# Kernel tuning notes

Hardware: AMD Instinct MI355X
Metric: run time of the kernel (lower is better)

## Reference

```python
import jax, jax.numpy as jnp
import numpy as np

Q_H, KV_H, DIM = 32, 8, 4096
HEAD_DIM = DIM // Q_H
FACTOR = Q_H // KV_H
BS, SL = 2, 2048


def setup_inputs() -> dict:
    key = jax.random.key(0)
    ks = jax.random.split(key, 9)
    s_in = 1.0 / np.sqrt(DIM)
    x = jax.random.normal(ks[0], (BS, SL, DIM), dtype=jnp.float32)
    wq_w = jax.random.uniform(ks[1], (DIM, Q_H * HEAD_DIM), jnp.float32, -s_in, s_in)
    wq_b = jax.random.uniform(ks[2], (Q_H * HEAD_DIM,), jnp.float32, -s_in, s_in)
    wk_w = jax.random.uniform(ks[3], (DIM, KV_H * HEAD_DIM), jnp.float32, -s_in, s_in)
    wk_b = jax.random.uniform(ks[4], (KV_H * HEAD_DIM,), jnp.float32, -s_in, s_in)
    wv_w = jax.random.uniform(ks[5], (DIM, KV_H * HEAD_DIM), jnp.float32, -s_in, s_in)
    wv_b = jax.random.uniform(ks[6], (KV_H * HEAD_DIM,), jnp.float32, -s_in, s_in)
    wo_w = jax.random.uniform(ks[7], (DIM, DIM), jnp.float32, -s_in, s_in)
    wo_b = jax.random.uniform(ks[8], (DIM,), jnp.float32, -s_in, s_in)
    return {"x": x, "wq_w": wq_w, "wq_b": wq_b, "wk_w": wk_w, "wk_b": wk_b,
            "wv_w": wv_w, "wv_b": wv_b, "wo_w": wo_w, "wo_b": wo_b}


def reference(x, wq_w, wq_b, wk_w, wk_b, wv_w, wv_b, wo_w, wo_b):
    bs, sl, _ = x.shape
    # projections
    q = (x @ wq_w + wq_b).reshape(bs, sl, Q_H, HEAD_DIM)          # [b,s,Hq,d]
    k = (x @ wk_w + wk_b).reshape(bs, sl, KV_H, HEAD_DIM)         # [b,s,Hkv,d]
    v = (x @ wv_w + wv_b).reshape(bs, sl, KV_H, HEAD_DIM)
    # group queries by kv head: [b,s,Hkv,factor,d]
    qg = q.reshape(bs, sl, KV_H, FACTOR, HEAD_DIM)
    scale = 1.0 / jnp.sqrt(jnp.asarray(HEAD_DIM, x.dtype))
    # scores: broadcast kv heads instead of physically repeating
    attn = jnp.einsum('bqhfd,bkhd->bhfqk', qg, k) * scale          # [b,Hkv,f,Sq,Sk]
    att = jax.nn.softmax(attn, axis=-1)
    a = jnp.einsum('bhfqk,bkhd->bqhfd', att, v)                    # [b,Sq,Hkv,f,d]
    a = a.reshape(bs, sl, DIM)
    return a @ wo_w + wo_b
```

## Files before the change

kernel.cpp:

```cpp
#include <hip/hip_runtime.h>
#include <math.h>


typedef unsigned short u16;
typedef unsigned int u32;
typedef __bf16 bf16x8 __attribute__((ext_vector_type(8)));
typedef float f32x4 __attribute__((ext_vector_type(4)));
typedef float f32x16 __attribute__((ext_vector_type(16)));
typedef unsigned short u16x8 __attribute__((ext_vector_type(8)));
typedef unsigned short u16x4 __attribute__((ext_vector_type(4)));
typedef int i32x2 __attribute__((ext_vector_type(2)));

#define MFMA16(a, b, c) __builtin_amdgcn_mfma_f32_16x16x32_bf16((a), (b), (c), 0, 0, 0)
#define MFMA32(a, b, c) __builtin_amdgcn_mfma_f32_32x32x16_bf16((a), (b), (c), 0, 0, 0)

#define GLDS(gp, lp)                                                      \
  __builtin_amdgcn_global_load_lds(                                       \
      (const __attribute__((address_space(1))) unsigned int*)(gp),        \
      (__attribute__((address_space(3))) unsigned int*)(lp), 16, 0, 0)

__device__ __forceinline__ u16 f2b(float f) {
  unsigned b = __float_as_uint(f);
  b += 0x7fffu + ((b >> 16) & 1u);
  return (u16)(b >> 16);
}

__device__ __forceinline__ u32 pk2(float a, float b) {
  union { __bf16 h[2]; u32 w; } u;
  u.h[0] = (__bf16)a;
  u.h[1] = (__bf16)b;
  return u.w;
}

__global__ __launch_bounds__(256) void cast_f32_bf16(const float* __restrict__ in,
                                                     u16* __restrict__ out, int n) {
  int i = (blockIdx.x * 256 + threadIdx.x) * 8;
  if (i >= n) return;
  f32x4 a = *(const f32x4*)&in[i];
  f32x4 b = *(const f32x4*)&in[i + 4];
  u16x8 v;
#pragma unroll
  for (int j = 0; j < 4; j++) { v[j] = f2b(a[j]); v[4 + j] = f2b(b[j]); }
  *(u16x8*)&out[i] = v;
}

__global__ __launch_bounds__(256) void transpose_cast(const float* __restrict__ in,
                                                      u16* __restrict__ out,
                                                      int R, int C) {
  __shared__ u16 t[32][33];
  const int lc = threadIdx.x & 31;
  const int lr = threadIdx.x >> 5;
  const int c0 = blockIdx.x * 32, r0 = blockIdx.y * 32;
#pragma unroll
  for (int i = 0; i < 4; i++) {
    int r = lr + i * 8;
    t[r][lc] = f2b(in[(size_t)(r0 + r) * C + c0 + lc]);
  }
  __syncthreads();
#pragma unroll
  for (int i = 0; i < 4; i++) {
    int r = lr + i * 8;
    out[(size_t)(c0 + r) * R + r0 + lc] = t[lc][r];
  }
}

template <int STORE_T, int OUT_F32>
__global__ __launch_bounds__(256, 2) void gemm_bt(const u16* __restrict__ A,
                                                  const u16* __restrict__ BT,
                                                  const float* __restrict__ bias,
                                                  void* __restrict__ Cv,
                                                  int M, int N) {
  __shared__ u16 As[128][64];
  __shared__ u16 Bs[128][64];
  const int tid = threadIdx.x;
  const int lane = tid & 63, wave = tid >> 6;
  const int l15 = lane & 15, quad = lane >> 4;
  const int m0 = blockIdx.y * 128, n0 = blockIdx.x * 128;
  const int wm = (wave >> 1) * 64, wn = (wave & 1) * 64;
  const int srow = wave * 32 + (lane >> 3);
  const int scol = (lane & 7) * 8;
  const u16* gA = &A[(size_t)(m0 + srow) * 4096 + scol];
  const u16* gB = &BT[(size_t)(n0 + srow) * 4096 + scol];
  f32x4 acc[4][4] = {};
  for (int kb = 0; kb < 4096; kb += 64) {
    __syncthreads();
#pragma unroll
    for (int j = 0; j < 4; j++) {
      GLDS(gA + (size_t)j * 8 * 4096 + kb, &As[wave * 32 + j * 8][0]);
      GLDS(gB + (size_t)j * 8 * 4096 + kb, &Bs[wave * 32 + j * 8][0]);
    }
    __syncthreads();
#pragma unroll
    for (int ks = 0; ks < 2; ks++) {
      bf16x8 a[4], b[4];
#pragma unroll
      for (int mt = 0; mt < 4; mt++)
        a[mt] = *(const bf16x8*)&As[wm + mt * 16 + l15][ks * 32 + quad * 8];
#pragma unroll
      for (int nt = 0; nt < 4; nt++)
        b[nt] = *(const bf16x8*)&Bs[wn + nt * 16 + l15][ks * 32 + quad * 8];
#pragma unroll
      for (int mt = 0; mt < 4; mt++)
#pragma unroll
        for (int nt = 0; nt < 4; nt++)
          acc[mt][nt] = MFMA16(a[mt], b[nt], acc[mt][nt]);
    }
  }
  float bv[4];
#pragma unroll
  for (int nt = 0; nt < 4; nt++) bv[nt] = bias[n0 + wn + nt * 16 + l15];
#pragma unroll
  for (int mt = 0; mt < 4; mt++) {
    const int row = m0 + wm + mt * 16 + quad * 4;
#pragma unroll
    for (int nt = 0; nt < 4; nt++) {
      const int col = n0 + wn + nt * 16 + l15;
      if (STORE_T) {
        u16x4 v;
#pragma unroll
        for (int r = 0; r < 4; r++) v[r] = f2b(acc[mt][nt][r] + bv[nt]);
        *(u16x4*)&((u16*)Cv)[(size_t)col * M + row] = v;
      } else if (OUT_F32) {
#pragma unroll
        for (int r = 0; r < 4; r++)
          ((float*)Cv)[(size_t)(row + r) * N + col] = acc[mt][nt][r] + bv[nt];
      } else {
#pragma unroll
        for (int r = 0; r < 4; r++)
          ((u16*)Cv)[(size_t)(row + r) * N + col] = f2b(acc[mt][nt][r] + bv[nt]);
      }
    }
  }
}

#define STAGE_K(bf, t)                                                         \
  {                                                                            \
    _Pragma("unroll") for (int i_ = 0; i_ < 4; i_++)                           \
      GLDS(gK + (size_t)((t) * 64 + i_ * 4) * 1024 + (offK ^ ((i_ & 1) << 5)), \
           &KsB[bf][(wave * 16 + i_ * 4) * 128]);                              \
  }
#define STAGE_V(t)                                                             \
  {                                                                            \
    _Pragma("unroll") for (int i_ = 0; i_ < 4; i_++)                           \
      GLDS(gV + (size_t)(i_ * 8) * 4096 + (t) * 64,                            \
           &Vs[(wave * 32 + i_ * 8) * 64]);                                    \
  }

__global__ __launch_bounds__(256, 3) void flash_gqa(const u16* __restrict__ K,
                                                    const u16* __restrict__ VT,
                                                    u16* __restrict__ QO) {
  __shared__ __align__(16) u16 KsB[2][64 * 128];
  __shared__ __align__(16) u16 Vs[128 * 64];
  const int tid = threadIdx.x;
  const int lane = tid & 63, wave = tid >> 6;
  const int l31 = lane & 31, hi = lane >> 5;
  const int bx = blockIdx.x;
  const int qt = bx & 15, h = (bx >> 4) & 31, b = bx >> 9;
  const int hk = h >> 2;
  const int qrow0 = b * 2048 + qt * 128 + wave * 32;
  const float scl2 = 0.08838834764831845f * 1.4426950408889634f;

  const int offK = ((lane & 15) * 8) ^ ((lane >> 4) << 3);
  const u16* gK = &K[(size_t)(b * 2048 + wave * 16 + (lane >> 4)) * 1024 + hk * 128];
  const u16* gV = &VT[(size_t)(hk * 128 + wave * 32 + (lane >> 3)) * 4096 + b * 2048 +
                      (((lane & 7) * 8) ^ ((lane >> 3) << 3))];

  STAGE_K(0, 0);

  bf16x8 qf[8];
#pragma unroll
  for (int ks = 0; ks < 8; ks++)
    qf[ks] = *(const bf16x8*)&QO[(size_t)(qrow0 + l31) * 4096 + h * 128 + ks * 16 + hi * 8];

  f32x16 o[4] = {};
  float mrun = -3.0e38f, lrun = 0.0f;

  __syncthreads();

  for (int t = 0; t < 32; t++) {
    const int bf = t & 1;
    STAGE_V(t);
    if (t < 31) STAGE_K(bf ^ 1, t + 1);

    f32x16 st[2] = {};
    __builtin_amdgcn_s_setprio(1);
#pragma unroll
    for (int ks = 0; ks < 8; ks++) {
#pragma unroll
      for (int kvt = 0; kvt < 2; kvt++) {
        const int row = kvt * 32 + l31;
        bf16x8 kf = *(const bf16x8*)&KsB[bf][row * 128 +
                                            ((ks * 16 + hi * 8) ^ ((row & 7) << 3))];
        st[kvt] = MFMA32(kf, qf[ks], st[kvt]);
      }
    }
    __builtin_amdgcn_s_setprio(0);

    float m8[8];
#pragma unroll
    for (int r = 0; r < 8; r++)
      m8[r] = fmaxf(fmaxf(fmaxf(st[0][r], st[0][r + 8]), st[1][r]), st[1][r + 8]);
    float mA = fmaxf(fmaxf(m8[0], m8[1]), m8[2]);
    mA = fmaxf(fmaxf(mA, m8[3]), m8[4]);
    mA = fmaxf(fmaxf(mA, m8[5]), m8[6]);
    mA = fmaxf(mA, m8[7]);
    i32x2 mr = __builtin_amdgcn_permlane32_swap(__float_as_int(mA), __float_as_int(mA),
                                                false, false);
    const float mx = fmaxf(__int_as_float(mr[0]), __int_as_float(mr[1]));
    const float mxs = mx * scl2;
    if (__any(mxs > mrun + 8.0f)) {
      const float mn = fmaxf(mrun, mxs);
      const float alpha = __builtin_amdgcn_exp2f(mrun - mn);
      mrun = mn;
      lrun *= alpha;
#pragma unroll
      for (int re = 0; re < 16; re++) {
        const float av = __shfl(alpha, (re & 3) + 8 * (re >> 2) + 4 * hi, 64);
#pragma unroll
        for (int dt = 0; dt < 4; dt++) o[dt][re] *= av;
      }
    }
    float rsa[4] = {0.f, 0.f, 0.f, 0.f};
#pragma unroll
    for (int kvt = 0; kvt < 2; kvt++)
#pragma unroll
      for (int r = 0; r < 16; r++) {
        const float p = __builtin_amdgcn_exp2f(fmaf(st[kvt][r], scl2, -mrun));
        st[kvt][r] = p;
        rsa[r & 3] += p;
      }
    float rs = (rsa[0] + rsa[1]) + (rsa[2] + rsa[3]);
    i32x2 rr = __builtin_amdgcn_permlane32_swap(__float_as_int(rs), __float_as_int(rs),
                                                false, false);
    lrun += __int_as_float(rr[0]) + __int_as_float(rr[1]);

    u32 W0[8], W1[8];
#pragma unroll
    for (int rp = 0; rp < 8; rp++) {
      W0[rp] = pk2(st[0][2 * rp], st[0][2 * rp + 1]);
      W1[rp] = pk2(st[1][2 * rp], st[1][2 * rp + 1]);
    }
    u32 fw[4][4];
#pragma unroll
    for (int kvs = 0; kvs < 4; kvs++) {
#pragma unroll
      for (int sl = 0; sl < 2; sl++) {
        const u32 wa = (kvs < 2) ? W0[4 * (kvs & 1) + sl] : W1[4 * (kvs & 1) + sl];
        const u32 wb = (kvs < 2) ? W0[4 * (kvs & 1) + 2 + sl] : W1[4 * (kvs & 1) + 2 + sl];
        i32x2 r = __builtin_amdgcn_permlane32_swap((int)wa, (int)wb, false, false);
        fw[kvs][sl] = (u32)r[0];
        fw[kvs][2 + sl] = (u32)r[1];
      }
    }

    __syncthreads();

    __builtin_amdgcn_s_setprio(1);
#pragma unroll
    for (int kvs = 0; kvs < 4; kvs++) {
      union { u32 w[4]; bf16x8 v; } pa;
      pa.w[0] = fw[kvs][0]; pa.w[1] = fw[kvs][1];
      pa.w[2] = fw[kvs][2]; pa.w[3] = fw[kvs][3];
#pragma unroll
      for (int dt = 0; dt < 4; dt++) {
        const int row = dt * 32 + l31;
        bf16x8 vf = *(const bf16x8*)&Vs[row * 64 +
                                        ((kvs * 16 + hi * 8) ^ ((row & 7) << 3))];
        o[dt] = MFMA32(pa.v, vf, o[dt]);
      }
    }
    __builtin_amdgcn_s_setprio(0);

    __syncthreads();
  }

  const float invl = 1.0f / lrun;
#pragma unroll
  for (int re = 0; re < 16; re++) {
    const int qv = (re & 3) + 8 * (re >> 2) + 4 * hi;
    const float il = __shfl(invl, qv, 64);
    const size_t rowb = (size_t)(qrow0 + qv) * 4096 + h * 128;
#pragma unroll
    for (int dt = 0; dt < 4; dt++)
      QO[rowb + dt * 32 + l31] = f2b(o[dt][re] * il);
  }
}

extern "C" void kernel_launch(void* const* d_in, const int* in_sizes, int n_in,
                              void* d_out, int out_size, void* d_ws, size_t ws_size,
                              hipStream_t stream) {
  (void)in_sizes; (void)n_in; (void)out_size; (void)ws_size;
  const float* x    = (const float*)d_in[0];
  const float* wq_w = (const float*)d_in[1];
  const float* wq_b = (const float*)d_in[2];
  const float* wk_w = (const float*)d_in[3];
  const float* wk_b = (const float*)d_in[4];
  const float* wv_w = (const float*)d_in[5];
  const float* wv_b = (const float*)d_in[6];
  const float* wo_w = (const float*)d_in[7];
  const float* wo_b = (const float*)d_in[8];
  float* out = (float*)d_out;
  char* ws = (char*)d_ws;
  char* od = (char*)d_out;

  u16* TQ  = (u16*)(ws);
  u16* QA  = (u16*)(ws + 33554432);
  u16* Xb  = (u16*)(od);
  u16* TK  = (u16*)(od + 33554432);
  u16* TV  = (u16*)(od + 41943040);
  u16* Kb  = (u16*)(od + 50331648);
  u16* VTb = (u16*)(od + 58720256);

  cast_f32_bf16<<<8192, 256, 0, stream>>>(x, Xb, 16777216);
  transpose_cast<<<dim3(128, 128), 256, 0, stream>>>(wq_w, TQ, 4096, 4096);
  transpose_cast<<<dim3(32, 128), 256, 0, stream>>>(wk_w, TK, 4096, 1024);
  transpose_cast<<<dim3(32, 128), 256, 0, stream>>>(wv_w, TV, 4096, 1024);

  gemm_bt<0, 0><<<dim3(32, 32), 256, 0, stream>>>(Xb, TQ, wq_b, QA, 4096, 4096);
  gemm_bt<0, 0><<<dim3(8, 32), 256, 0, stream>>>(Xb, TK, wk_b, Kb, 4096, 1024);
  gemm_bt<1, 0><<<dim3(8, 32), 256, 0, stream>>>(Xb, TV, wv_b, VTb, 4096, 1024);

  transpose_cast<<<dim3(128, 128), 256, 0, stream>>>(wo_w, TQ, 4096, 4096);

  flash_gqa<<<dim3(1024), 256, 0, stream>>>(Kb, VTb, QA);

  gemm_bt<0, 1><<<dim3(32, 32), 256, 0, stream>>>(QA, TQ, wo_b, out, 4096, 4096);
}
```

Baseline: 876.5 us.

## Software-pipeline PV matmul one tile behind QK with triple-buffered V

Restructures the flash-attention loop so the P·V MFMAs for tile t-1 run right after the QK MFMAs for tile t. This removes one of the two __syncthreads per iteration and lets softmax work overlap with matrix-core work. V becomes triple-buffered and is prefetched a tile ahead along with K. Shared-memory offsets are precomputed into registers and block indices are remapped for cache locality. The cost is larger LDS and register use, with launch bounds dropped from 3 to 2 blocks per CU, so occupancy falls.

```diff
diff --git a/kernel.cpp b/kernel.cpp
--- a/kernel.cpp
+++ b/kernel.cpp
@@ -133,28 +133,43 @@
   }
 }
 
-#define STAGE_K(bf, t)                                                         \
+#define STAGE_K(kb, tt)                                                        \
   {                                                                            \
     _Pragma("unroll") for (int i_ = 0; i_ < 4; i_++)                           \
-      GLDS(gK + (size_t)((t) * 64 + i_ * 4) * 1024 + (offK ^ ((i_ & 1) << 5)), \
-           &KsB[bf][(wave * 16 + i_ * 4) * 128]);                              \
-  }
-#define STAGE_V(t)                                                             \
+      GLDS(gK + (size_t)((tt) * 64 + i_ * 4) * 1024 + (offK ^ ((i_ & 1) << 5)),\
+           &KsF[(kb) * 8192 + (wave * 16 + i_ * 4) * 128]);                    \
+  }
+#define STAGE_V(vb, tt)                                                        \
   {                                                                            \
     _Pragma("unroll") for (int i_ = 0; i_ < 4; i_++)                           \
-      GLDS(gV + (size_t)(i_ * 8) * 4096 + (t) * 64,                            \
-           &Vs[(wave * 32 + i_ * 8) * 64]);                                    \
-  }
-
-__global__ __launch_bounds__(256, 3) void flash_gqa(const u16* __restrict__ K,
+      GLDS(gV + (size_t)(i_ * 8) * 4096 + (tt) * 64,                           \
+           &VsF[(vb) * 8192 + (wave * 32 + i_ * 8) * 64]);                     \
+  }
+
+#define PV_STEP(pb)                                                            \
+  {                                                                            \
+    __builtin_amdgcn_s_setprio(1);                                             \
+    _Pragma("unroll") for (int kvs = 0; kvs < 4; kvs++) {                      \
+      union { u32 w[4]; bf16x8 v; } pa;                                        \
+      pa.w[0] = fw[kvs][0]; pa.w[1] = fw[kvs][1];                              \
+      pa.w[2] = fw[kvs][2]; pa.w[3] = fw[kvs][3];                              \
+      _Pragma("unroll") for (int dt = 0; dt < 4; dt++) {                       \
+        bf16x8 vf = *(const bf16x8*)&VsF[(pb) * 8192 + vOff[dt][kvs]];         \
+        o[dt] = MFMA32(pa.v, vf, o[dt]);                                       \
+      }                                                                        \
+    }                                                                          \
+    __builtin_amdgcn_s_setprio(0);                                             \
+  }
+
+__global__ __launch_bounds__(256, 2) void flash_gqa(const u16* __restrict__ K,
                                                     const u16* __restrict__ VT,
                                                     u16* __restrict__ QO) {
-  __shared__ __align__(16) u16 KsB[2][64 * 128];
-  __shared__ __align__(16) u16 Vs[128 * 64];
+  __shared__ __align__(16) u16 KsF[2 * 64 * 128];
+  __shared__ __align__(16) u16 VsF[3 * 128 * 64];
   const int tid = threadIdx.x;
   const int lane = tid & 63, wave = tid >> 6;
   const int l31 = lane & 31, hi = lane >> 5;
-  const int bx = blockIdx.x;
+  const int bx = (blockIdx.x & 7) * 128 + (blockIdx.x >> 3);
   const int qt = bx & 15, h = (bx >> 4) & 31, b = bx >> 9;
   const int hk = h >> 2;
   const int qrow0 = b * 2048 + qt * 128 + wave * 32;
@@ -165,7 +180,24 @@
   const u16* gV = &VT[(size_t)(hk * 128 + wave * 32 + (lane >> 3)) * 4096 + b * 2048 +
                       (((lane & 7) * 8) ^ ((lane >> 3) << 3))];
 
+  int kOff[2][8], vOff[4][4];
+#pragma unroll
+  for (int kvt = 0; kvt < 2; kvt++) {
+    const int row = kvt * 32 + l31;
+#pragma unroll
+    for (int ks = 0; ks < 8; ks++)
+      kOff[kvt][ks] = row * 128 + ((ks * 16 + hi * 8) ^ ((row & 7) << 3));
+  }
+#pragma unroll
+  for (int dt = 0; dt < 4; dt++) {
+    const int row = dt * 32 + l31;
+#pragma unroll
+    for (int kvs = 0; kvs < 4; kvs++)
+      vOff[dt][kvs] = row * 64 + ((kvs * 16 + hi * 8) ^ ((row & 7) << 3));
+  }
+
   STAGE_K(0, 0);
+  STAGE_V(0, 0);
 
   bf16x8 qf[8];
 #pragma unroll
@@ -174,13 +206,16 @@
 
   f32x16 o[4] = {};
   float mrun = -3.0e38f, lrun = 0.0f;
+  u32 fw[4][4];
 
   __syncthreads();
 
   for (int t = 0; t < 32; t++) {
-    const int bf = t & 1;
-    STAGE_V(t);
-    if (t < 31) STAGE_K(bf ^ 1, t + 1);
+    const int kb = t & 1;
+    if (t < 31) {
+      STAGE_K(kb ^ 1, t + 1);
+      STAGE_V((t + 1) % 3, t + 1);
+    }
 
     f32x16 st[2] = {};
     __builtin_amdgcn_s_setprio(1);
@@ -188,13 +223,13 @@
     for (int ks = 0; ks < 8; ks++) {
 #pragma unroll
       for (int kvt = 0; kvt < 2; kvt++) {
-        const int row = kvt * 32 + l31;
-        bf16x8 kf = *(const bf16x8*)&KsB[bf][row * 128 +
-                                            ((ks * 16 + hi * 8) ^ ((row & 7) << 3))];
+        bf16x8 kf = *(const bf16x8*)&KsF[kb * 8192 + kOff[kvt][ks]];
         st[kvt] = MFMA32(kf, qf[ks], st[kvt]);
       }
     }
     __builtin_amdgcn_s_setprio(0);
+
+    if (t > 0) PV_STEP((t - 1) % 3);
 
     float m8[8];
 #pragma unroll
@@ -240,7 +275,6 @@
       W0[rp] = pk2(st[0][2 * rp], st[0][2 * rp + 1]);
       W1[rp] = pk2(st[1][2 * rp], st[1][2 * rp + 1]);
     }
-    u32 fw[4][4];
 #pragma unroll
     for (int kvs = 0; kvs < 4; kvs++) {
 #pragma unroll
@@ -254,25 +288,9 @@
     }
 
     __syncthreads();
-
-    __builtin_amdgcn_s_setprio(1);
-#pragma unroll
-    for (int kvs = 0; kvs < 4; kvs++) {
-      union { u32 w[4]; bf16x8 v; } pa;
-      pa.w[0] = fw[kvs][0]; pa.w[1] = fw[kvs][1];
-      pa.w[2] = fw[kvs][2]; pa.w[3] = fw[kvs][3];
-#pragma unroll
-      for (int dt = 0; dt < 4; dt++) {
-        const int row = dt * 32 + l31;
-        bf16x8 vf = *(const bf16x8*)&Vs[row * 64 +
-                                        ((kvs * 16 + hi * 8) ^ ((row & 7) << 3))];
-        o[dt] = MFMA32(pa.v, vf, o[dt]);
-      }
-    }
-    __builtin_amdgcn_s_setprio(0);
-
-    __syncthreads();
-  }
+  }
+
+  PV_STEP(1);
 
   const float invl = 1.0f / lrun;
 #pragma unroll
```

After: 857.4 us. 1.02x faster.
